# Kernel tuning notes

Measured on AMD Instinct MI355X. Metric: run time of the kernel, lower is better.

## Reference

```python
import jax, jax.numpy as jnp
import numpy as np

N_HEADS = 16
THETA = 10000.0


def _rope_cos_sin(seq_len, head_dim):
    # freqs_cis = exp(i * pos * theta^(-2j/d)), shape (seq_len, head_dim//2)
    inv_freq = 1.0 / (THETA ** (np.arange(0, head_dim, 2, dtype=np.float32) / head_dim))
    ang = np.arange(seq_len, dtype=np.float32)[:, None] * inv_freq[None, :]
    return jnp.asarray(np.cos(ang)), jnp.asarray(np.sin(ang))


def _apply_rope(t, cos, sin):
    # t: [B, S, H, hd]; rotate consecutive pairs as complex numbers
    B, S, H, hd = t.shape
    pairs = t.reshape(B, S, H, hd // 2, 2)
    r, i = pairs[..., 0], pairs[..., 1]
    c = cos[None, :, None, :]  # [1, S, 1, hd//2]
    s = sin[None, :, None, :]
    out_r = r * c - i * s
    out_i = r * s + i * c
    return jnp.stack([out_r, out_i], axis=-1).reshape(B, S, H, hd)


def setup_inputs() -> dict:
    key = jax.random.key(0)
    ks = jax.random.split(key, 5)
    B, S, D = 2, 2048, 2048
    scale = 1.0 / np.sqrt(D)
    return {
        "x": jax.random.normal(ks[0], (B, S, D), dtype=jnp.float32),
        "wq": jax.random.normal(ks[1], (D, D), dtype=jnp.float32) * scale,
        "wk": jax.random.normal(ks[2], (D, D), dtype=jnp.float32) * scale,
        "wv": jax.random.normal(ks[3], (D, D), dtype=jnp.float32) * scale,
        "wo": jax.random.normal(ks[4], (D, D), dtype=jnp.float32) * scale,
    }


def reference(x, wq, wk, wv, wo):
    B, S, D = x.shape
    H = N_HEADS
    hd = D // H
    cos, sin = _rope_cos_sin(S, hd)

    xq = (x @ wq.T).reshape(B, S, H, hd)
    xk = (x @ wk.T).reshape(B, S, H, hd)
    xv = (x @ wv.T).reshape(B, S, H, hd)

    xq = _apply_rope(xq, cos, sin)
    xk = _apply_rope(xk, cos, sin)

    # [B, H, S, S] scores, full (non-causal) softmax as in the source
    scores = jnp.einsum("bqhd,bkhd->bhqk", xq, xk) / jnp.sqrt(jnp.float32(hd))
    attn = jax.nn.softmax(scores, axis=-1)
    out = jnp.einsum("bhqk,bkhd->bqhd", attn, xv).reshape(B, S, D)
    return out @ wo.T
```

## Files before the change

kernel.cpp:

```cpp
#include <hip/hip_runtime.h>
#include <hip/hip_bf16.h>
#include <stdint.h>


typedef __attribute__((ext_vector_type(4))) float f32x4;
typedef __attribute__((ext_vector_type(8))) short bf16x8;

typedef __attribute__((address_space(3))) unsigned int lds_u32;
typedef __attribute__((address_space(1))) const unsigned int gbl_u32;

__device__ __forceinline__ void async16(const void* g, void* l) {
  __builtin_amdgcn_global_load_lds((gbl_u32*)g, (lds_u32*)l, 16, 0, 0);
}

__device__ __forceinline__ float bf_to_f(unsigned short u) {
  union { unsigned int i; float f; } v; v.i = ((unsigned int)u) << 16; return v.f;
}
__device__ __forceinline__ unsigned short f_to_bf(float f) {
  union { float f; unsigned int i; } v; v.f = f;
  unsigned int r = v.i + 0x7FFFu + ((v.i >> 16) & 1u);
  return (unsigned short)(r >> 16);
}
__device__ __forceinline__ unsigned int cvt_pk_bf16(float lo, float hi) {
  unsigned int r;
  asm("v_cvt_pk_bf16_f32 %0, %1, %2" : "=v"(r) : "v"(lo), "v"(hi));
  return r;
}

#define B_ 2
#define S_ 2048
#define D_ 2048
#define H_ 16
#define HD_ 128
#define KVB 128

__global__ __launch_bounds__(256) void conv_all(const float* __restrict__ x,
                                                const float* __restrict__ wq,
                                                const float* __restrict__ wk,
                                                const float* __restrict__ wv,
                                                const float* __restrict__ wo,
                                                unsigned short* __restrict__ xb,
                                                unsigned short* __restrict__ wb) {
  int i = blockIdx.x * 256 + threadIdx.x;
  const float* s;
  unsigned short* d;
  int off;
  if (i < 2097152) {
    s = x; d = xb; off = i;
  } else {
    int j = i - 2097152;
    int t = j >> 20;
    off = j & 1048575;
    s = (t == 0) ? wq : (t == 1) ? wk : (t == 2) ? wv : wo;
    d = wb + (size_t)t * 4194304;
  }
  float4 v = ((const float4*)s)[off];
  uint2 o;
  o.x = (unsigned int)f_to_bf(v.x) | ((unsigned int)f_to_bf(v.y) << 16);
  o.y = (unsigned int)f_to_bf(v.z) | ((unsigned int)f_to_bf(v.w) << 16);
  ((uint2*)d)[off] = o;
}

__global__ __launch_bounds__(256) void rope_table_kernel(float* __restrict__ cosT,
                                                         float* __restrict__ sinT) {
  int i = blockIdx.x * 256 + threadIdx.x;
  int s = i >> 6, j = i & 63;
  float inv = powf(10000.0f, -(float)(2 * j) * (1.0f / 128.0f));
  float ang = (float)s * inv;
  float sv, cv;
  sincosf(ang, &sv, &cv);
  cosT[i] = cv;
  sinT[i] = sv;
}

__global__ __launch_bounds__(256, 2) void qkv_gemm(const unsigned short* __restrict__ A,
                                                   const unsigned short* __restrict__ W,
                                                   unsigned short* __restrict__ Qb,
                                                   unsigned short* __restrict__ Kb,
                                                   unsigned short* __restrict__ Vtb,
                                                   const float* __restrict__ cosT,
                                                   const float* __restrict__ sinT) {
  __shared__ unsigned short sA[2][128 * 64];
  __shared__ unsigned short sB[2][128 * 64];
  const int K = 2048, N = 2048;
  const int tid = threadIdx.x;
  const int l = tid & 63, wv = tid >> 6;
  const int lane15 = l & 15, lhi = l >> 4;
  const int wm = wv >> 1, wn = wv & 1;
  const int bm = blockIdx.x, bn = blockIdx.y;
  const int sector = bn >> 4, bnl = bn & 15;

  const int srow = tid >> 3;
  const int colD = (tid & 7) << 4;
  const unsigned short* aSrc[4];
  const unsigned short* bSrc[4];
  unsigned int lofs[4];
#pragma unroll
  for (int i = 0; i < 4; i++) {
    int row = i * 32 + srow;
    int cS = colD ^ ((row & 7) << 4);
    aSrc[i] = A + (size_t)(bm * 128 + row) * K + (cS >> 1);
    bSrc[i] = W + (size_t)(bn * 128 + row) * K + (cS >> 1);
    lofs[i] = row * 128 + colD;
  }

  f32x4 acc[4][4];
  const f32x4 zero = {0.f, 0.f, 0.f, 0.f};
#pragma unroll
  for (int i = 0; i < 4; i++)
#pragma unroll
    for (int j = 0; j < 4; j++) acc[i][j] = zero;

#pragma unroll
  for (int i = 0; i < 4; i++) {
    async16(aSrc[i], (char*)&sA[0][0] + lofs[i]); aSrc[i] += 64;
    async16(bSrc[i], (char*)&sB[0][0] + lofs[i]); bSrc[i] += 64;
  }

  for (int t = 0; t < 32; ++t) {
    const int cur = t & 1;
    __syncthreads();
    if (t < 31) {
#pragma unroll
      for (int i = 0; i < 4; i++) {
        async16(aSrc[i], (char*)&sA[cur ^ 1][0] + lofs[i]); aSrc[i] += 64;
        async16(bSrc[i], (char*)&sB[cur ^ 1][0] + lofs[i]); bSrc[i] += 64;
      }
    }
    const char* sAc = (const char*)&sA[cur][0];
    const char* sBc = (const char*)&sB[cur][0];

#pragma unroll
    for (int h = 0; h < 2; h++) {
      bf16x8 af[4], bfr[4];
#pragma unroll
      for (int i = 0; i < 4; i++) {
        int row = wm * 64 + i * 16 + lane15;
        af[i] = *(const bf16x8*)(sAc + row * 128 +
                                 ((h * 64 + lhi * 16) ^ ((row & 7) << 4)));
      }
#pragma unroll
      for (int j = 0; j < 4; j++) {
        int row = wn * 64 + j * 16 + lane15;
        bfr[j] = *(const bf16x8*)(sBc + row * 128 +
                                  ((h * 64 + lhi * 16) ^ ((row & 7) << 4)));
      }
      __builtin_amdgcn_s_setprio(1);
#pragma unroll
      for (int i = 0; i < 4; i++)
#pragma unroll
        for (int j = 0; j < 4; j++)
          acc[i][j] = __builtin_amdgcn_mfma_f32_16x16x32_bf16(af[i], bfr[j], acc[i][j], 0, 0, 0);
      __builtin_amdgcn_s_setprio(0);
    }
  }

#pragma unroll
  for (int i = 0; i < 4; i++) {
    int m0 = bm * 128 + wm * 64 + i * 16 + lhi * 4;
#pragma unroll
    for (int j = 0; j < 4; j++) {
      int n = bnl * 128 + wn * 64 + j * 16 + lane15;
      if (sector == 0) {
#pragma unroll
        for (int r = 0; r < 4; r++) Qb[(size_t)(m0 + r) * N + n] = f_to_bf(acc[i][j][r]);
      } else if (sector == 1) {
        int s0 = m0 & (S_ - 1);
        int jp = (n & (HD_ - 1)) >> 1;
        int odd = n & 1;
#pragma unroll
        for (int r = 0; r < 4; r++) {
          float own = acc[i][j][r];
          float prt = __shfl_xor(own, 1);
          float c = cosT[(s0 + r) * 64 + jp];
          float sn = sinT[(s0 + r) * 64 + jp];
          float outv = odd ? fmaf(prt, sn, own * c) : own * c - prt * sn;
          Kb[(size_t)(m0 + r) * N + n] = f_to_bf(outv);
        }
      } else {
        int s0 = m0 & (S_ - 1);
        size_t row = (size_t)((m0 >> 11) * D_ + n);
        uint2 st;
        st.x = (unsigned int)f_to_bf(acc[i][j][0]) | ((unsigned int)f_to_bf(acc[i][j][1]) << 16);
        st.y = (unsigned int)f_to_bf(acc[i][j][2]) | ((unsigned int)f_to_bf(acc[i][j][3]) << 16);
        *(uint2*)(Vtb + row * S_ + s0) = st;
      }
    }
  }
}

__global__ __launch_bounds__(256, 2) void gemm_out(const unsigned short* __restrict__ A,
                                                   const unsigned short* __restrict__ Bm,
                                                   float* __restrict__ Cf) {
  __shared__ unsigned short sA[2][128 * 64];
  __shared__ unsigned short sB[2][128 * 64];
  const int K = 2048, N = 2048;
  const int tid = threadIdx.x;
  const int l = tid & 63, wv = tid >> 6;
  const int lane15 = l & 15, lhi = l >> 4;
  const int wm = wv >> 1, wn = wv & 1;
  const int bm = blockIdx.x, bn = blockIdx.y;

  const int srow = tid >> 3;
  const int colD = (tid & 7) << 4;
  const unsigned short* aSrc[4];
  const unsigned short* bSrc[4];
  unsigned int lofs[4];
#pragma unroll
  for (int i = 0; i < 4; i++) {
    int row = i * 32 + srow;
    int cS = colD ^ ((row & 7) << 4);
    aSrc[i] = A + (size_t)(bm * 128 + row) * K + (cS >> 1);
    bSrc[i] = Bm + (size_t)(bn * 128 + row) * K + (cS >> 1);
    lofs[i] = row * 128 + colD;
  }

  f32x4 acc[4][4];
  const f32x4 zero = {0.f, 0.f, 0.f, 0.f};
#pragma unroll
  for (int i = 0; i < 4; i++)
#pragma unroll
    for (int j = 0; j < 4; j++) acc[i][j] = zero;

#pragma unroll
  for (int i = 0; i < 4; i++) {
    async16(aSrc[i], (char*)&sA[0][0] + lofs[i]); aSrc[i] += 64;
    async16(bSrc[i], (char*)&sB[0][0] + lofs[i]); bSrc[i] += 64;
  }

  for (int t = 0; t < 32; ++t) {
    const int cur = t & 1;
    __syncthreads();
    if (t < 31) {
#pragma unroll
      for (int i = 0; i < 4; i++) {
        async16(aSrc[i], (char*)&sA[cur ^ 1][0] + lofs[i]); aSrc[i] += 64;
        async16(bSrc[i], (char*)&sB[cur ^ 1][0] + lofs[i]); bSrc[i] += 64;
      }
    }
    const char* sAc = (const char*)&sA[cur][0];
    const char* sBc = (const char*)&sB[cur][0];

#pragma unroll
    for (int h = 0; h < 2; h++) {
      bf16x8 af[4], bfr[4];
#pragma unroll
      for (int i = 0; i < 4; i++) {
        int row = wm * 64 + i * 16 + lane15;
        af[i] = *(const bf16x8*)(sAc + row * 128 +
                                 ((h * 64 + lhi * 16) ^ ((row & 7) << 4)));
      }
#pragma unroll
      for (int j = 0; j < 4; j++) {
        int row = wn * 64 + j * 16 + lane15;
        bfr[j] = *(const bf16x8*)(sBc + row * 128 +
                                  ((h * 64 + lhi * 16) ^ ((row & 7) << 4)));
      }
      __builtin_amdgcn_s_setprio(1);
#pragma unroll
      for (int i = 0; i < 4; i++)
#pragma unroll
        for (int j = 0; j < 4; j++)
          acc[i][j] = __builtin_amdgcn_mfma_f32_16x16x32_bf16(af[i], bfr[j], acc[i][j], 0, 0, 0);
      __builtin_amdgcn_s_setprio(0);
    }
  }

#pragma unroll
  for (int i = 0; i < 4; i++) {
    int m0 = bm * 128 + wm * 64 + i * 16 + lhi * 4;
#pragma unroll
    for (int j = 0; j < 4; j++) {
      int n = bn * 128 + wn * 64 + j * 16 + lane15;
#pragma unroll
      for (int r = 0; r < 4; r++) Cf[(size_t)(m0 + r) * N + n] = acc[i][j][r];
    }
  }
}

__global__ __launch_bounds__(512, 2) void attn_kernel(const unsigned short* __restrict__ Q,
                                                      const unsigned short* __restrict__ K,
                                                      const unsigned short* __restrict__ Vt,
                                                      unsigned short* __restrict__ ctx,
                                                      const float* __restrict__ cosT,
                                                      const float* __restrict__ sinT) {
  __shared__ unsigned short sK[2][KVB * 128];
  __shared__ unsigned short sV[2][128 * KVB];
  const int tid = threadIdx.x, l = tid & 63, w = tid >> 6;
  const int lane15 = l & 15, lhi = l >> 4;
  const int bh = blockIdx.x * 4 + (blockIdx.y >> 3);
  const int qt = blockIdx.y & 7;
  const int b = bh >> 4, h = bh & 15;
  const int q0 = qt * 256;
  const unsigned short* Kg = K + ((size_t)(b * S_)) * D_ + h * HD_;
  const unsigned short* Vg = Vt + ((size_t)bh * HD_) * S_;
  const float qscale = 0.08838834764831845f * 1.44269504f;
  const float THR = 11.5415603f;

  const unsigned short* gp[8];
  unsigned int lofs[8];
  size_t gstep;
  if (w < 4) {
#pragma unroll
    for (int i = 0; i < 8; i++) {
      int row = w * 32 + i * 4 + (l >> 4);
      int colD = (l & 15) << 4;
      int colS = colD ^ ((row & 7) << 4);
      gp[i] = Kg + (size_t)row * D_ + (colS >> 1);
      lofs[i] = row * 256 + colD;
    }
    gstep = (size_t)KVB * D_;
  } else {
#pragma unroll
    for (int i = 0; i < 8; i++) {
      int row = (w - 4) * 32 + i * 4 + (l >> 4);
      int colD = (l & 15) << 4;
      int colS = colD ^ ((row & 7) << 4);
      gp[i] = Vg + (size_t)row * S_ + (colS >> 1);
      lofs[i] = row * 256 + colD;
    }
    gstep = KVB;
  }

  bf16x8 qf[2][4];
#pragma unroll
  for (int s = 0; s < 2; s++) {
    int s_q = q0 + w * 32 + s * 16 + lane15;
    const unsigned short* Qrow = Q + ((size_t)(b * S_ + s_q)) * D_ + h * HD_;
#pragma unroll
    for (int kc = 0; kc < 4; kc++) {
      int d0 = kc * 32 + lhi * 8;
      uint4 raw = *(const uint4*)(Qrow + d0);
      float4 cv = *(const float4*)(cosT + (size_t)s_q * 64 + (d0 >> 1));
      float4 sv = *(const float4*)(sinT + (size_t)s_q * 64 + (d0 >> 1));
      unsigned int u[4] = {raw.x, raw.y, raw.z, raw.w};
      float cc[4] = {cv.x, cv.y, cv.z, cv.w};
      float ss[4] = {sv.x, sv.y, sv.z, sv.w};
      unsigned int o[4];
#pragma unroll
      for (int p = 0; p < 4; p++) {
        float re = bf_to_f((unsigned short)(u[p] & 0xffffu));
        float im = bf_to_f((unsigned short)(u[p] >> 16));
        float orr = (re * cc[p] - im * ss[p]) * qscale;
        float oi = (re * ss[p] + im * cc[p]) * qscale;
        o[p] = (unsigned int)f_to_bf(orr) | ((unsigned int)f_to_bf(oi) << 16);
      }
      union { uint4 u4; bf16x8 v; } cvt;
      cvt.u4.x = o[0]; cvt.u4.y = o[1]; cvt.u4.z = o[2]; cvt.u4.w = o[3];
      qf[s][kc] = cvt.v;
    }
  }

  float mrun[2] = {-1e30f, -1e30f}, lrun[2] = {0.f, 0.f};
  const f32x4 zero = {0.f, 0.f, 0.f, 0.f};
  f32x4 oacc[2][8];
#pragma unroll
  for (int s = 0; s < 2; s++)
#pragma unroll
    for (int nf = 0; nf < 8; nf++) oacc[s][nf] = zero;

  {
    char* base = (w < 4) ? (char*)&sK[0][0] : (char*)&sV[0][0];
#pragma unroll
    for (int i = 0; i < 8; i++) { async16(gp[i], base + lofs[i]); gp[i] += gstep; }
  }

  for (int t = 0; t < S_ / KVB; ++t) {
    const int cur = t & 1;
    __syncthreads();
    if (t < S_ / KVB - 1) {
      char* base = (w < 4) ? (char*)&sK[cur ^ 1][0] : (char*)&sV[cur ^ 1][0];
#pragma unroll
      for (int i = 0; i < 8; i++) { async16(gp[i], base + lofs[i]); gp[i] += gstep; }
    }
    const unsigned short* sKc = sK[cur];
    const unsigned short* sVc = sV[cur];

    f32x4 sacc[2][8];
#pragma unroll
    for (int s = 0; s < 2; s++)
#pragma unroll
      for (int n = 0; n < 8; n++) sacc[s][n] = zero;
    __builtin_amdgcn_s_setprio(1);
#pragma unroll
    for (int n = 0; n < 8; n++) {
      int row = n * 16 + lane15;
#pragma unroll
      for (int kc = 0; kc < 4; kc++) {
        bf16x8 kf = *(const bf16x8*)((const char*)sKc + row * 256 +
                                     ((kc * 64 + lhi * 16) ^ ((row & 7) << 4)));
        sacc[0][n] = __builtin_amdgcn_mfma_f32_16x16x32_bf16(kf, qf[0][kc], sacc[0][n], 0, 0, 0);
        sacc[1][n] = __builtin_amdgcn_mfma_f32_16x16x32_bf16(kf, qf[1][kc], sacc[1][n], 0, 0, 0);
      }
    }
    __builtin_amdgcn_s_setprio(0);

    float pmax[2];
#pragma unroll
    for (int s = 0; s < 2; s++) {
      float mn[8];
#pragma unroll
      for (int n = 0; n < 8; n++)
        mn[n] = fmaxf(fmaxf(sacc[s][n][0], sacc[s][n][1]), fmaxf(sacc[s][n][2], sacc[s][n][3]));
      float pm = fmaxf(fmaxf(fmaxf(mn[0], mn[1]), fmaxf(mn[2], mn[3])),
                       fmaxf(fmaxf(mn[4], mn[5]), fmaxf(mn[6], mn[7])));
      pm = fmaxf(pm, __shfl_xor(pm, 16));
      pm = fmaxf(pm, __shfl_xor(pm, 32));
      pmax[s] = pm;
    }
    if (!__all(fmaxf(pmax[0] - mrun[0], pmax[1] - mrun[1]) <= THR)) {
#pragma unroll
      for (int s = 0; s < 2; s++) {
        float mnew = fmaxf(mrun[s], pmax[s]);
        float alpha = exp2f(mrun[s] - mnew);
        lrun[s] *= alpha;
        float af[4];
#pragma unroll
        for (int r = 0; r < 4; r++) af[r] = __shfl(alpha, lhi * 4 + r);
#pragma unroll
        for (int nf = 0; nf < 8; nf++)
#pragma unroll
          for (int r = 0; r < 4; r++) oacc[s][nf][r] *= af[r];
        mrun[s] = mnew;
      }
    }
    bf16x8 paS[2][4];
#pragma unroll
    for (int s = 0; s < 2; s++) {
      float rs = 0.f;
      unsigned int wlo[8], whi[8];
#pragma unroll
      for (int n = 0; n < 8; n++) {
        float p0 = exp2f(sacc[s][n][0] - mrun[s]);
        float p1 = exp2f(sacc[s][n][1] - mrun[s]);
        float p2 = exp2f(sacc[s][n][2] - mrun[s]);
        float p3 = exp2f(sacc[s][n][3] - mrun[s]);
        rs += (p0 + p1) + (p2 + p3);
        wlo[n] = cvt_pk_bf16(p0, p1);
        whi[n] = cvt_pk_bf16(p2, p3);
      }
      rs += __shfl_xor(rs, 16);
      rs += __shfl_xor(rs, 32);
      lrun[s] += rs;
#pragma unroll
      for (int kc = 0; kc < 4; kc++) {
        unsigned int A = wlo[2 * kc], Bw = whi[2 * kc];
        unsigned int C = wlo[2 * kc + 1], Dw = whi[2 * kc + 1];
        asm("v_permlane32_swap_b32 %0, %1" : "+v"(A), "+v"(C));
        asm("v_permlane16_swap_b32 %0, %1" : "+v"(A), "+v"(C));
        asm("v_permlane32_swap_b32 %0, %1" : "+v"(Bw), "+v"(Dw));
        asm("v_permlane16_swap_b32 %0, %1" : "+v"(Bw), "+v"(Dw));
        union { uint4 u4; bf16x8 v; } pk;
        pk.u4.x = A; pk.u4.y = Bw; pk.u4.z = C; pk.u4.w = Dw;
        paS[s][kc] = pk.v;
      }
    }

    __builtin_amdgcn_s_setprio(1);
#pragma unroll
    for (int nf = 0; nf < 8; nf++) {
      int row = nf * 16 + lane15;
#pragma unroll
      for (int kc = 0; kc < 4; kc++) {
        bf16x8 vf = *(const bf16x8*)((const char*)sVc + row * 256 +
                                     ((kc * 64 + lhi * 16) ^ ((row & 7) << 4)));
        oacc[0][nf] = __builtin_amdgcn_mfma_f32_16x16x32_bf16(paS[0][kc], vf, oacc[0][nf], 0, 0, 0);
        oacc[1][nf] = __builtin_amdgcn_mfma_f32_16x16x32_bf16(paS[1][kc], vf, oacc[1][nf], 0, 0, 0);
      }
    }
    __builtin_amdgcn_s_setprio(0);
  }

#pragma unroll
  for (int s = 0; s < 2; s++) {
    float inv = 1.0f / lrun[s];
    float invr[4];
#pragma unroll
    for (int r = 0; r < 4; r++) invr[r] = __shfl(inv, lhi * 4 + r);
    unsigned short* Og = ctx + ((size_t)(b * S_ + q0 + w * 32 + s * 16)) * D_ + h * HD_;
#pragma unroll
    for (int r = 0; r < 4; r++) {
      int qrow = lhi * 4 + r;
#pragma unroll
      for (int nf = 0; nf < 8; nf++)
        Og[(size_t)qrow * D_ + nf * 16 + lane15] = f_to_bf(oacc[s][nf][r] * invr[r]);
    }
  }
}

extern "C" void kernel_launch(void* const* d_in, const int* in_sizes, int n_in,
                              void* d_out, int out_size, void* d_ws, size_t ws_size,
                              hipStream_t stream) {
  (void)in_sizes; (void)n_in; (void)out_size; (void)ws_size;
  const float* x = (const float*)d_in[0];
  const float* wq = (const float*)d_in[1];
  const float* wk = (const float*)d_in[2];
  const float* wv = (const float*)d_in[3];
  const float* wo = (const float*)d_in[4];
  float* out = (float*)d_out;

  char* ws = (char*)d_ws;
  const size_t MB = 1024 * 1024;
  unsigned short* xb  = (unsigned short*)(ws + 0 * MB);
  unsigned short* wqb = (unsigned short*)(ws + 16 * MB);
  unsigned short* wob = (unsigned short*)(ws + 40 * MB);
  unsigned short* Qb  = (unsigned short*)(ws + 48 * MB);
  unsigned short* Kb  = (unsigned short*)(ws + 64 * MB);
  unsigned short* Vtb = (unsigned short*)(ws + 80 * MB);
  float* cosT = (float*)(ws + 96 * MB);
  float* sinT = (float*)(ws + 96 * MB + 524288);
  unsigned short* ctxb = xb;

  const int M = B_ * S_;

  conv_all<<<24576, 256, 0, stream>>>(x, wq, wk, wv, wo, xb, wqb);
  rope_table_kernel<<<512, 256, 0, stream>>>(cosT, sinT);

  qkv_gemm<<<dim3(M / 128, 48), 256, 0, stream>>>(xb, wqb, Qb, Kb, Vtb, cosT, sinT);

  attn_kernel<<<dim3(8, 32), 512, 0, stream>>>(Qb, Kb, Vtb, ctxb, cosT, sinT);

  gemm_out<<<dim3(M / 128, D_ / 128), 256, 0, stream>>>(ctxb, wob, out);
}
```

Measured before the change: 267.5 us.

## Restructure GEMM and attention main loops with counted vmcnt waits; fuse rope table into conversion

Replaces the per-iteration __syncthreads double-buffer loop in both GEMMs and the attention kernel with a two-stage prefetch: both buffers are issued up front, and each step waits with s_waitcnt vmcnt(8) so only the older stage must land before compute. Refills are issued right after compute, leaving one load batch in flight during compute. The rope cos/sin table kernel is folded into the conversion kernel as extra blocks, removing one launch. The hand-written vmcnt counts must match the number of async loads per thread, or correctness breaks.

```diff
diff --git a/kernel.cpp b/kernel.cpp
--- a/kernel.cpp
+++ b/kernel.cpp
@@ -40,8 +40,21 @@
                                                 const float* __restrict__ wv,
                                                 const float* __restrict__ wo,
                                                 unsigned short* __restrict__ xb,
-                                                unsigned short* __restrict__ wb) {
+                                                unsigned short* __restrict__ wb,
+                                                float* __restrict__ cosT,
+                                                float* __restrict__ sinT) {
   int i = blockIdx.x * 256 + threadIdx.x;
+  if (i >= 6291456) {
+    int j = i - 6291456;
+    int s = j >> 6, jj = j & 63;
+    float inv = powf(10000.0f, -(float)(2 * jj) * (1.0f / 128.0f));
+    float ang = (float)s * inv;
+    float sv, cv;
+    sincosf(ang, &sv, &cv);
+    cosT[j] = cv;
+    sinT[j] = sv;
+    return;
+  }
   const float* s;
   unsigned short* d;
   int off;
@@ -59,18 +72,6 @@
   o.x = (unsigned int)f_to_bf(v.x) | ((unsigned int)f_to_bf(v.y) << 16);
   o.y = (unsigned int)f_to_bf(v.z) | ((unsigned int)f_to_bf(v.w) << 16);
   ((uint2*)d)[off] = o;
-}
-
-__global__ __launch_bounds__(256) void rope_table_kernel(float* __restrict__ cosT,
-                                                         float* __restrict__ sinT) {
-  int i = blockIdx.x * 256 + threadIdx.x;
-  int s = i >> 6, j = i & 63;
-  float inv = powf(10000.0f, -(float)(2 * j) * (1.0f / 128.0f));
-  float ang = (float)s * inv;
-  float sv, cv;
-  sincosf(ang, &sv, &cv);
-  cosT[i] = cv;
-  sinT[i] = sv;
 }
 
 __global__ __launch_bounds__(256, 2) void qkv_gemm(const unsigned short* __restrict__ A,
@@ -111,25 +112,16 @@
 #pragma unroll
     for (int j = 0; j < 4; j++) acc[i][j] = zero;
 
-#pragma unroll
-  for (int i = 0; i < 4; i++) {
-    async16(aSrc[i], (char*)&sA[0][0] + lofs[i]); aSrc[i] += 64;
-    async16(bSrc[i], (char*)&sB[0][0] + lofs[i]); bSrc[i] += 64;
-  }
-
-  for (int t = 0; t < 32; ++t) {
-    const int cur = t & 1;
-    __syncthreads();
-    if (t < 31) {
-#pragma unroll
-      for (int i = 0; i < 4; i++) {
-        async16(aSrc[i], (char*)&sA[cur ^ 1][0] + lofs[i]); aSrc[i] += 64;
-        async16(bSrc[i], (char*)&sB[cur ^ 1][0] + lofs[i]); bSrc[i] += 64;
-      }
-    }
-    const char* sAc = (const char*)&sA[cur][0];
-    const char* sBc = (const char*)&sB[cur][0];
-
+  auto stage = [&](int slot) {
+#pragma unroll
+    for (int i = 0; i < 4; i++) {
+      async16(aSrc[i], (char*)&sA[slot][0] + lofs[i]); aSrc[i] += 64;
+      async16(bSrc[i], (char*)&sB[slot][0] + lofs[i]); bSrc[i] += 64;
+    }
+  };
+  auto compute = [&](int slot) {
+    const char* sAc = (const char*)&sA[slot][0];
+    const char* sBc = (const char*)&sB[slot][0];
 #pragma unroll
     for (int h = 0; h < 2; h++) {
       bf16x8 af[4], bfr[4];
@@ -153,7 +145,24 @@
           acc[i][j] = __builtin_amdgcn_mfma_f32_16x16x32_bf16(af[i], bfr[j], acc[i][j], 0, 0, 0);
       __builtin_amdgcn_s_setprio(0);
     }
-  }
+  };
+
+  stage(0);
+  stage(1);
+
+  for (int t = 0; t < 30; ++t) {
+    asm volatile("s_waitcnt vmcnt(8)" ::: "memory");
+    __builtin_amdgcn_s_barrier();
+    compute(t & 1);
+    __builtin_amdgcn_s_barrier();
+    stage(t & 1);
+  }
+  asm volatile("s_waitcnt vmcnt(8)" ::: "memory");
+  __builtin_amdgcn_s_barrier();
+  compute(0);
+  asm volatile("s_waitcnt vmcnt(0)" ::: "memory");
+  __builtin_amdgcn_s_barrier();
+  compute(1);
 
 #pragma unroll
   for (int i = 0; i < 4; i++) {
@@ -222,25 +231,16 @@
 #pragma unroll
     for (int j = 0; j < 4; j++) acc[i][j] = zero;
 
-#pragma unroll
-  for (int i = 0; i < 4; i++) {
-    async16(aSrc[i], (char*)&sA[0][0] + lofs[i]); aSrc[i] += 64;
-    async16(bSrc[i], (char*)&sB[0][0] + lofs[i]); bSrc[i] += 64;
-  }
-
-  for (int t = 0; t < 32; ++t) {
-    const int cur = t & 1;
-    __syncthreads();
-    if (t < 31) {
-#pragma unroll
-      for (int i = 0; i < 4; i++) {
-        async16(aSrc[i], (char*)&sA[cur ^ 1][0] + lofs[i]); aSrc[i] += 64;
-        async16(bSrc[i], (char*)&sB[cur ^ 1][0] + lofs[i]); bSrc[i] += 64;
-      }
-    }
-    const char* sAc = (const char*)&sA[cur][0];
-    const char* sBc = (const char*)&sB[cur][0];
-
+  auto stage = [&](int slot) {
+#pragma unroll
+    for (int i = 0; i < 4; i++) {
+      async16(aSrc[i], (char*)&sA[slot][0] + lofs[i]); aSrc[i] += 64;
+      async16(bSrc[i], (char*)&sB[slot][0] + lofs[i]); bSrc[i] += 64;
+    }
+  };
+  auto compute = [&](int slot) {
+    const char* sAc = (const char*)&sA[slot][0];
+    const char* sBc = (const char*)&sB[slot][0];
 #pragma unroll
     for (int h = 0; h < 2; h++) {
       bf16x8 af[4], bfr[4];
@@ -264,7 +264,23 @@
           acc[i][j] = __builtin_amdgcn_mfma_f32_16x16x32_bf16(af[i], bfr[j], acc[i][j], 0, 0, 0);
       __builtin_amdgcn_s_setprio(0);
     }
-  }
+  };
+
+  stage(0);
+  stage(1);
+  for (int t = 0; t < 30; ++t) {
+    asm volatile("s_waitcnt vmcnt(8)" ::: "memory");
+    __builtin_amdgcn_s_barrier();
+    compute(t & 1);
+    __builtin_amdgcn_s_barrier();
+    stage(t & 1);
+  }
+  asm volatile("s_waitcnt vmcnt(8)" ::: "memory");
+  __builtin_amdgcn_s_barrier();
+  compute(0);
+  asm volatile("s_waitcnt vmcnt(0)" ::: "memory");
+  __builtin_amdgcn_s_barrier();
+  compute(1);
 
 #pragma unroll
   for (int i = 0; i < 4; i++) {
@@ -359,22 +375,15 @@
 #pragma unroll
     for (int nf = 0; nf < 8; nf++) oacc[s][nf] = zero;
 
-  {
-    char* base = (w < 4) ? (char*)&sK[0][0] : (char*)&sV[0][0];
+  auto stage = [&](int slot) {
+    char* base = (w < 4) ? (char*)&sK[slot][0] : (char*)&sV[slot][0];
 #pragma unroll
     for (int i = 0; i < 8; i++) { async16(gp[i], base + lofs[i]); gp[i] += gstep; }
-  }
-
-  for (int t = 0; t < S_ / KVB; ++t) {
-    const int cur = t & 1;
-    __syncthreads();
-    if (t < S_ / KVB - 1) {
-      char* base = (w < 4) ? (char*)&sK[cur ^ 1][0] : (char*)&sV[cur ^ 1][0];
-#pragma unroll
-      for (int i = 0; i < 8; i++) { async16(gp[i], base + lofs[i]); gp[i] += gstep; }
-    }
-    const unsigned short* sKc = sK[cur];
-    const unsigned short* sVc = sV[cur];
+  };
+
+  auto compute = [&](int slot) {
+    const unsigned short* sKc = sK[slot];
+    const unsigned short* sVc = sV[slot];
 
     f32x4 sacc[2][8];
 #pragma unroll
@@ -469,7 +478,24 @@
       }
     }
     __builtin_amdgcn_s_setprio(0);
-  }
+  };
+
+  stage(0);
+  stage(1);
+
+  for (int t = 0; t < 14; ++t) {
+    asm volatile("s_waitcnt vmcnt(8)" ::: "memory");
+    __builtin_amdgcn_s_barrier();
+    compute(t & 1);
+    __builtin_amdgcn_s_barrier();
+    stage(t & 1);
+  }
+  asm volatile("s_waitcnt vmcnt(8)" ::: "memory");
+  __builtin_amdgcn_s_barrier();
+  compute(0);
+  asm volatile("s_waitcnt vmcnt(0)" ::: "memory");
+  __builtin_amdgcn_s_barrier();
+  compute(1);
 
 #pragma unroll
   for (int s = 0; s < 2; s++) {
@@ -513,8 +539,7 @@
 
   const int M = B_ * S_;
 
-  conv_all<<<24576, 256, 0, stream>>>(x, wq, wk, wv, wo, xb, wqb);
-  rope_table_kernel<<<512, 256, 0, stream>>>(cosT, sinT);
+  conv_all<<<25088, 256, 0, stream>>>(x, wq, wk, wv, wo, xb, wqb, cosT, sinT);
 
   qkv_gemm<<<dim3(M / 128, 48), 256, 0, stream>>>(xb, wqb, Qb, Kb, Vtb, cosT, sinT);
 
```

New measurement: 293.7 us. 1.1x slower.
